# Kernel optimization log

Measured on AMD Instinct MI355X. Metric: run time of the kernel, lower is better.

## Reference

```python
import jax, jax.numpy as jnp
import numpy as np

B, D, NH, HD, L, P, FF = 2, 256, 8, 32, 4, 4, 1024
SPATIAL = np.array([[100, 100], [50, 50], [25, 25], [13, 13]], dtype=np.int64)
S_TOTAL = int(SPATIAL.prod(1).sum())  # 13294
EPS = 1e-5


def setup_inputs() -> dict:
    key = jax.random.key(0)
    ks = jax.random.split(key, 20)
    std = 0.02
    f32 = jnp.float32
    return {
        "query": jax.random.normal(ks[0], (B, S_TOTAL, D), f32),
        "query_pos": jax.random.normal(ks[1], (B, S_TOTAL, D), f32),
        "valid_ratios": jnp.ones((B, L, 2), f32),
        "spatial_shapes": SPATIAL,
        "level_start_index": np.concatenate([[0], SPATIAL.prod(1).cumsum()[:-1]]).astype(np.int64),
        "W_off": jax.random.normal(ks[2], (D, NH * L * P * 2), f32) * std,
        "b_off": jax.random.normal(ks[3], (NH * L * P * 2,), f32) * std,
        "W_attn": jax.random.normal(ks[4], (D, NH * L * P), f32) * std,
        "b_attn": jax.random.normal(ks[5], (NH * L * P,), f32) * std,
        "W_val": jax.random.normal(ks[6], (D, D), f32) * std,
        "b_val": jnp.zeros((D,), f32),
        "W_out": jax.random.normal(ks[7], (D, D), f32) * std,
        "b_out": jnp.zeros((D,), f32),
        "ln1_g": jnp.ones((D,), f32),
        "ln1_b": jnp.zeros((D,), f32),
        "W1": jax.random.normal(ks[8], (D, FF), f32) * std,
        "b1": jnp.zeros((FF,), f32),
        "W2": jax.random.normal(ks[9], (FF, D), f32) * std,
        "b2": jnp.zeros((D,), f32),
        "ln2_g": jnp.ones((D,), f32),
        "ln2_b": jnp.zeros((D,), f32),
    }


def _layer_norm(x, g, b):
    m = x.mean(-1, keepdims=True)
    v = ((x - m) ** 2).mean(-1, keepdims=True)
    return (x - m) * jax.lax.rsqrt(v + EPS) * g + b


def _bilinear_sample(v, loc, H, W):
    # v: [B, NH, H*W, HD]; loc: [B, NH, S, P, 2] normalized to [0,1]
    # Matches F.grid_sample(bilinear, padding_mode='zeros', align_corners=False)
    x = loc[..., 0] * W - 0.5
    y = loc[..., 1] * H - 0.5
    x0 = jnp.floor(x)
    y0 = jnp.floor(y)
    lx, ly = x - x0, y - y0
    x0i = x0.astype(jnp.int32)
    y0i = y0.astype(jnp.int32)
    x1i, y1i = x0i + 1, y0i + 1

    def corner(yi, xi, w):
        valid = (xi >= 0) & (xi < W) & (yi >= 0) & (yi < H)
        idx = jnp.clip(yi, 0, H - 1) * W + jnp.clip(xi, 0, W - 1)  # [B,NH,S,P]
        b_, h_, s_, p_ = idx.shape
        g = jnp.take_along_axis(v, idx.reshape(b_, h_, s_ * p_)[..., None], axis=2)
        g = g.reshape(b_, h_, s_, p_, -1)
        return g * (w * valid)[..., None]

    return (corner(y0i, x0i, (1 - lx) * (1 - ly)) + corner(y0i, x1i, lx * (1 - ly))
            + corner(y1i, x0i, (1 - lx) * ly) + corner(y1i, x1i, lx * ly))


def _forward(query, query_pos, valid_ratios, spatial_shapes,
             W_off, b_off, W_attn, b_attn, W_val, b_val, W_out, b_out,
             ln1_g, ln1_b, W1, b1, W2, b2, ln2_g, ln2_b):
    ss = np.asarray(spatial_shapes)
    Bq, S, _ = query.shape

    # ----- reference points (per-pixel centers, normalized by valid ratios) -----
    refs = []
    for lvl in range(ss.shape[0]):
        H, W = int(ss[lvl, 0]), int(ss[lvl, 1])
        ry, rx = jnp.meshgrid(jnp.linspace(0.5, H - 0.5, H), jnp.linspace(0.5, W - 0.5, W), indexing='ij')
        vy = valid_ratios[:, lvl, 1][:, None, None]
        vx = valid_ratios[:, lvl, 0][:, None, None]
        ry = ry[None] / (vy * H)
        rx = rx[None] / (vx * W)
        refs.append(jnp.stack((rx, ry), -1).reshape(Bq, H * W, 2))
    ref = jnp.concatenate(refs, 1)  # [B, S, 2] (identical across levels)

    # ----- multi-scale deformable attention -----
    q = query + query_pos
    v = (query @ W_val + b_val).reshape(Bq, S, NH, HD).transpose(0, 2, 1, 3)  # [B,NH,S,HD]
    off = (q @ W_off + b_off).reshape(Bq, S, NH, L, P, 2)
    aw = jax.nn.softmax((q @ W_attn + b_attn).reshape(Bq, S, NH, L * P), -1)
    aw = aw.reshape(Bq, S, NH, L, P)
    normalizer = jnp.asarray(ss[:, ::-1].copy(), jnp.float32)  # (W, H) per level
    loc = ref[:, :, None, None, None, :] + off / normalizer[None, None, None, :, None, :]  # [B,S,NH,L,P,2]

    starts = np.concatenate([[0], ss.prod(1).cumsum()[:-1]])
    out = jnp.zeros((Bq, NH, S, HD), query.dtype)
    for lvl in range(ss.shape[0]):
        H, W = int(ss[lvl, 0]), int(ss[lvl, 1])
        s0 = int(starts[lvl])
        v_l = v[:, :, s0:s0 + H * W]                       # [B,NH,HW,HD]
        loc_l = loc[:, :, :, lvl].transpose(0, 2, 1, 3, 4)  # [B,NH,S,P,2]
        samp = _bilinear_sample(v_l, loc_l, H, W)           # [B,NH,S,P,HD]
        w_l = aw[:, :, :, lvl].transpose(0, 2, 1, 3)        # [B,NH,S,P]
        out = out + (samp * w_l[..., None]).sum(3)
    attn_out = out.transpose(0, 2, 1, 3).reshape(Bq, S, D) @ W_out + b_out

    # ----- residual + LN + FFN + residual + LN -----
    x = _layer_norm(query + attn_out, ln1_g, ln1_b)
    f = jax.nn.relu(x @ W1 + b1) @ W2 + b2
    return _layer_norm(x + f, ln2_g, ln2_b)


def reference(query, query_pos, valid_ratios, spatial_shapes, level_start_index,
              W_off, b_off, W_attn, b_attn, W_val, b_val, W_out, b_out,
              ln1_g, ln1_b, W1, b1, W2, b2, ln2_g, ln2_b):
    return _forward(query, query_pos, valid_ratios, spatial_shapes,
                    W_off, b_off, W_attn, b_attn, W_val, b_val, W_out, b_out,
                    ln1_g, ln1_b, W1, b1, W2, b2, ln2_g, ln2_b)
```

## Files before the change

kernel.cpp:

```cpp
#include <hip/hip_runtime.h>
#include <math.h>

#define R_ROWS 26588
#define S_TOT  13294
#define NHEAD  8
#define NLVL   4
#define EPSF   1e-5f

typedef __attribute__((ext_vector_type(8))) short short8;
typedef __attribute__((ext_vector_type(4))) float f32x4;
typedef __attribute__((ext_vector_type(2))) float f32x2;
typedef unsigned short ushort_t;

__device__ __forceinline__ unsigned short f2bf(float f) {
    unsigned int u = __builtin_bit_cast(unsigned int, f);
    unsigned int r = (u + 0x7FFFu + ((u >> 16) & 1u)) >> 16;
    return (unsigned short)r;
}

__global__ __launch_bounds__(256) void transpose_all_kernel(
    const float* __restrict__ W_val, const float* __restrict__ W_off,
    const float* __restrict__ W_attn, const float* __restrict__ W_out,
    const float* __restrict__ W1, const float* __restrict__ W2,
    ushort_t* __restrict__ wt_val, ushort_t* __restrict__ wt_off,
    ushort_t* __restrict__ wt_attn, ushort_t* __restrict__ wt_out,
    ushort_t* __restrict__ wt_w1, ushort_t* __restrict__ wt_w2)
{
    int bid = blockIdx.x;
    const float* src; ushort_t* dst; int K, N, t;
    if (bid < 64)       { src = W_val;  dst = wt_val;  K = 256;  N = 256;  t = bid; }
    else if (bid < 128) { src = W_off;  dst = wt_off;  K = 256;  N = 256;  t = bid - 64; }
    else if (bid < 160) { src = W_attn; dst = wt_attn; K = 256;  N = 128;  t = bid - 128; }
    else if (bid < 224) { src = W_out;  dst = wt_out;  K = 256;  N = 256;  t = bid - 160; }
    else if (bid < 480) { src = W1;     dst = wt_w1;   K = 256;  N = 1024; t = bid - 224; }
    else                { src = W2;     dst = wt_w2;   K = 1024; N = 256;  t = bid - 480; }
    int nt = N / 32;
    int bn = (t % nt) * 32, bk = (t / nt) * 32;

    __shared__ ushort_t tt[32][33];
    int x = threadIdx.x & 31;
    int y = threadIdx.x >> 5;
#pragma unroll
    for (int i = 0; i < 4; ++i) {
        int k = y + i * 8;
        tt[x][k] = f2bf(src[(long)(bk + k) * N + bn + x]);
    }
    __syncthreads();
#pragma unroll
    for (int i = 0; i < 4; ++i) {
        int n = y + i * 8;
        dst[(long)(bn + n) * K + bk + x] = tt[n][x];
    }
}

__global__ __launch_bounds__(256) void addcvt_kernel(
    const float* __restrict__ q, const float* __restrict__ p,
    ushort_t* __restrict__ qry_bf, ushort_t* __restrict__ qsum_bf, int n4)
{
    int i = blockIdx.x * 256 + threadIdx.x;
    if (i >= n4) return;
    float4 a = ((const float4*)q)[i];
    float4 b = ((const float4*)p)[i];
    uint2 qa, qs;
    qa.x = (unsigned)f2bf(a.x) | ((unsigned)f2bf(a.y) << 16);
    qa.y = (unsigned)f2bf(a.z) | ((unsigned)f2bf(a.w) << 16);
    qs.x = (unsigned)f2bf(a.x + b.x) | ((unsigned)f2bf(a.y + b.y) << 16);
    qs.y = (unsigned)f2bf(a.z + b.z) | ((unsigned)f2bf(a.w + b.w) << 16);
    ((uint2*)qry_bf)[i] = qa;
    ((uint2*)qsum_bf)[i] = qs;
}

__device__ __forceinline__ void gemm_body(
    ushort_t (*As)[40], ushort_t (*Bs)[40],
    const ushort_t* __restrict__ A, const ushort_t* __restrict__ Wt,
    const float* __restrict__ bias, void* __restrict__ Cv,
    int M, int N, int K, int bm, int bn, bool out_bf16, bool relu)
{
    const int tid  = threadIdx.x;
    const int wave = tid >> 6;
    const int lane = tid & 63;
    const int l15  = lane & 15;
    const int quad = lane >> 4;
    const int wm   = (wave >> 1) * 64;
    const int wn   = (wave & 1) * 64;
    const int kq   = (tid & 3) * 8;
    const int r0   = tid >> 2;

    f32x4 acc[4][4];
#pragma unroll
    for (int i = 0; i < 4; ++i)
#pragma unroll
        for (int j = 0; j < 4; ++j) acc[i][j] = (f32x4)0.0f;

    for (int k0 = 0; k0 < K; k0 += 32) {
#pragma unroll
        for (int i = 0; i < 2; ++i) {
            int r = r0 + i * 64;
            int m = bm + r;
            uint4 val; val.x = val.y = val.z = val.w = 0u;
            if (m < M) val = *(const uint4*)&A[(long)m * K + k0 + kq];
            *(uint4*)&As[r][kq] = val;
        }
#pragma unroll
        for (int i = 0; i < 2; ++i) {
            int n = r0 + i * 64;
            *(uint4*)&Bs[n][kq] = *(const uint4*)&Wt[(long)(bn + n) * K + k0 + kq];
        }
        __syncthreads();

        short8 af[4], bf[4];
#pragma unroll
        for (int mi = 0; mi < 4; ++mi)
            af[mi] = *(const short8*)&As[wm + mi * 16 + l15][quad * 8];
#pragma unroll
        for (int ni = 0; ni < 4; ++ni)
            bf[ni] = *(const short8*)&Bs[wn + ni * 16 + l15][quad * 8];
#pragma unroll
        for (int mi = 0; mi < 4; ++mi)
#pragma unroll
            for (int ni = 0; ni < 4; ++ni)
                acc[mi][ni] = __builtin_amdgcn_mfma_f32_16x16x32_bf16(
                    af[mi], bf[ni], acc[mi][ni], 0, 0, 0);
        __syncthreads();
    }

#pragma unroll
    for (int mi = 0; mi < 4; ++mi) {
#pragma unroll
        for (int r = 0; r < 4; ++r) {
            int row = bm + wm + mi * 16 + quad * 4 + r;
            if (row >= M) continue;
#pragma unroll
            for (int ni = 0; ni < 4; ++ni) {
                int col = bn + wn + ni * 16 + l15;
                float vv = acc[mi][ni][r] + bias[col];
                if (relu) vv = fmaxf(vv, 0.f);
                if (out_bf16)
                    ((ushort_t*)Cv)[(long)row * N + col] = f2bf(vv);
                else
                    ((float*)Cv)[(long)row * N + col] = vv;
            }
        }
    }
}

template<bool OUT_BF16, bool RELU>
__global__ __launch_bounds__(256) void gemm_mfma_kernel(
    const ushort_t* __restrict__ A, const ushort_t* __restrict__ Wt,
    const float* __restrict__ bias, void* __restrict__ Cv,
    int M, int N, int K)
{
    __shared__ ushort_t As[128][40];
    __shared__ ushort_t Bs[128][40];
    gemm_body(As, Bs, A, Wt, bias, Cv, M, N, K,
              blockIdx.x * 128, blockIdx.y * 128, OUT_BF16, RELU);
}

__global__ __launch_bounds__(256) void proj_kernel(
    const ushort_t* __restrict__ qry_bf, const ushort_t* __restrict__ q_bf,
    const ushort_t* __restrict__ wt_val, const ushort_t* __restrict__ wt_off,
    const ushort_t* __restrict__ wt_attn,
    const float* __restrict__ b_val, const float* __restrict__ b_off,
    const float* __restrict__ b_attn,
    ushort_t* __restrict__ v_bf, float* __restrict__ cb, float* __restrict__ logits)
{
    __shared__ ushort_t As[128][40];
    __shared__ ushort_t Bs[128][40];
    int y = blockIdx.y;
    const ushort_t* A; const ushort_t* Wt; const float* bias;
    void* C; bool outbf; int N, bn;
    if (y < 2)      { A = qry_bf; Wt = wt_val;  bias = b_val;  C = v_bf;   outbf = true;  N = 256; bn = y * 128; }
    else if (y < 4) { A = q_bf;   Wt = wt_off;  bias = b_off;  C = cb;     outbf = false; N = 256; bn = (y - 2) * 128; }
    else            { A = q_bf;   Wt = wt_attn; bias = b_attn; C = logits; outbf = false; N = 128; bn = 0; }
    gemm_body(As, Bs, A, Wt, bias, C, R_ROWS, N, 256, blockIdx.x * 128, bn, outbf, false);
}

__global__ __launch_bounds__(256) void deform_sample_kernel(
    const ushort_t* __restrict__ v, const float* __restrict__ off,
    const float* __restrict__ logits, const float* __restrict__ vr,
    ushort_t* __restrict__ out)
{
    const int Hs_[4] = {100, 50, 25, 13};
    const int S0_[4] = {0, 10000, 12500, 13125};

    int grp = blockIdx.x * 64 + (threadIdx.x >> 2);
    int j   = threadIdx.x & 3;
    if (grp >= R_ROWS * NHEAD) return;
    int h = grp & 7;
    int r = grp >> 3;
    int b = (r >= S_TOT) ? 1 : 0;
    int s = r - b * S_TOT;

    int lq = (s < 10000) ? 0 : (s < 12500) ? 1 : (s < 13125) ? 2 : 3;
    int t  = s - S0_[lq];
    int Wq = Hs_[lq];
    int iy = t / Wq;
    int jx = t - iy * Wq;
    float vx = vr[(b * NLVL + lq) * 2 + 0];
    float vy = vr[(b * NLVL + lq) * 2 + 1];
    float rx = (jx + 0.5f) / (vx * (float)Wq);
    float ry = (iy + 0.5f) / (vy * (float)Wq);

    const float* offp = off + (long)r * 256 + h * 32;
    float4 oa = ((const float4*)offp)[2 * j];
    float4 ob = ((const float4*)offp)[2 * j + 1];
    float4 lg = ((const float4*)(logits + (long)grp * 16))[j];

    float mx = fmaxf(fmaxf(lg.x, lg.y), fmaxf(lg.z, lg.w));
    mx = fmaxf(mx, __shfl_xor(mx, 1));
    mx = fmaxf(mx, __shfl_xor(mx, 2));
    float e0 = __expf(lg.x - mx), e1 = __expf(lg.y - mx);
    float e2 = __expf(lg.z - mx), e3 = __expf(lg.w - mx);
    float sum = e0 + e1 + e2 + e3;
    sum += __shfl_xor(sum, 1);
    sum += __shfl_xor(sum, 2);
    float inv = 1.f / sum;

    const int   H  = Hs_[j];
    const float fH = (float)H;
    const int   s0 = S0_[j];
    float oxs[4] = {oa.x, oa.z, ob.x, ob.z};
    float oys[4] = {oa.y, oa.w, ob.y, ob.w};
    float wts[4] = {e0 * inv, e1 * inv, e2 * inv, e3 * inv};
    float pw0[4], pw1[4], pw2[4], pw3[4];
    int   pi0[4], pi1[4], pi2[4], pi3[4];
#pragma unroll
    for (int i = 0; i < 4; ++i) {
        float x = rx * fH + oxs[i] - 0.5f;
        float y = ry * fH + oys[i] - 0.5f;
        float xf = floorf(x), yf = floorf(y);
        float lx = x - xf, ly = y - yf;
        int x0 = (int)xf, y0 = (int)yf;
        bool xv0 = (x0 >= 0) & (x0 < H);
        bool xv1 = (x0 >= -1) & (x0 < H - 1);
        bool yv0 = (y0 >= 0) & (y0 < H);
        bool yv1 = (y0 >= -1) & (y0 < H - 1);
        float w = wts[i];
        pw0[i] = (xv0 & yv0) ? (1.f - lx) * (1.f - ly) * w : 0.f;
        pw1[i] = (xv1 & yv0) ? lx * (1.f - ly) * w : 0.f;
        pw2[i] = (xv0 & yv1) ? (1.f - lx) * ly * w : 0.f;
        pw3[i] = (xv1 & yv1) ? lx * ly * w : 0.f;
        int xc0 = min(max(x0, 0), H - 1), xc1 = min(max(x0 + 1, 0), H - 1);
        int yc0 = min(max(y0, 0), H - 1), yc1 = min(max(y0 + 1, 0), H - 1);
        pi0[i] = s0 + yc0 * H + xc0;
        pi1[i] = s0 + yc0 * H + xc1;
        pi2[i] = s0 + yc1 * H + xc0;
        pi3[i] = s0 + yc1 * H + xc1;
    }

    const ushort_t* vb = v + ((long)b * S_TOT) * 256 + h * 32 + j * 8;
    f32x2 acc2[4];
#pragma unroll
    for (int c = 0; c < 4; ++c) acc2[c] = (f32x2)0.0f;

#define ACC_CORNER(IDX, WGT) do {                                            \
        uint4 g = *(const uint4*)&vb[(long)(IDX) * 256];                     \
        unsigned uu0 = g.x, uu1 = g.y, uu2 = g.z, uu3 = g.w;                 \
        f32x2 gv;                                                            \
        gv.x = __builtin_bit_cast(float, uu0 << 16);                         \
        gv.y = __builtin_bit_cast(float, uu0 & 0xFFFF0000u);                 \
        acc2[0] += gv * (WGT);                                               \
        gv.x = __builtin_bit_cast(float, uu1 << 16);                         \
        gv.y = __builtin_bit_cast(float, uu1 & 0xFFFF0000u);                 \
        acc2[1] += gv * (WGT);                                               \
        gv.x = __builtin_bit_cast(float, uu2 << 16);                         \
        gv.y = __builtin_bit_cast(float, uu2 & 0xFFFF0000u);                 \
        acc2[2] += gv * (WGT);                                               \
        gv.x = __builtin_bit_cast(float, uu3 << 16);                         \
        gv.y = __builtin_bit_cast(float, uu3 & 0xFFFF0000u);                 \
        acc2[3] += gv * (WGT);                                               \
    } while (0)

#pragma unroll
    for (int i = 0; i < 4; ++i) {
#pragma unroll
        for (int j2 = 0; j2 < 4; ++j2) {
            float w00 = __shfl(pw0[i], j2, 4);
            float w01 = __shfl(pw1[i], j2, 4);
            float w10 = __shfl(pw2[i], j2, 4);
            float w11 = __shfl(pw3[i], j2, 4);
            int   i00 = __shfl(pi0[i], j2, 4);
            int   i01 = __shfl(pi1[i], j2, 4);
            int   i10 = __shfl(pi2[i], j2, 4);
            int   i11 = __shfl(pi3[i], j2, 4);
            ACC_CORNER(i00, w00);
            ACC_CORNER(i01, w01);
            ACC_CORNER(i10, w10);
            ACC_CORNER(i11, w11);
        }
    }
#undef ACC_CORNER

    uint4 o;
    o.x = (unsigned)f2bf(acc2[0].x) | ((unsigned)f2bf(acc2[0].y) << 16);
    o.y = (unsigned)f2bf(acc2[1].x) | ((unsigned)f2bf(acc2[1].y) << 16);
    o.z = (unsigned)f2bf(acc2[2].x) | ((unsigned)f2bf(acc2[2].y) << 16);
    o.w = (unsigned)f2bf(acc2[3].x) | ((unsigned)f2bf(acc2[3].y) << 16);
    *(uint4*)&out[(long)r * 256 + h * 32 + j * 8] = o;
}

template<bool DUAL>
__global__ __launch_bounds__(256) void add_ln_kernel(
    const float* __restrict__ a, const float* __restrict__ b,
    const float* __restrict__ g, const float* __restrict__ beta,
    float* __restrict__ outf, ushort_t* __restrict__ outb)
{
    int row = blockIdx.x;
    int tid = threadIdx.x;
    float x = a[(long)row * 256 + tid] + b[(long)row * 256 + tid];
    float s1 = x, s2 = x * x;
#pragma unroll
    for (int o = 32; o > 0; o >>= 1) {
        s1 += __shfl_down(s1, o, 64);
        s2 += __shfl_down(s2, o, 64);
    }
    __shared__ float sh1[4], sh2[4];
    int w = tid >> 6;
    if ((tid & 63) == 0) { sh1[w] = s1; sh2[w] = s2; }
    __syncthreads();
    float t1 = sh1[0] + sh1[1] + sh1[2] + sh1[3];
    float t2 = sh2[0] + sh2[1] + sh2[2] + sh2[3];
    float mean = t1 * (1.f / 256.f);
    float var  = t2 * (1.f / 256.f) - mean * mean;
    float inv  = rsqrtf(var + EPSF);
    float y = (x - mean) * inv * g[tid] + beta[tid];
    outf[(long)row * 256 + tid] = y;
    if (DUAL) outb[(long)row * 256 + tid] = f2bf(y);
}

extern "C" void kernel_launch(void* const* d_in, const int* in_sizes, int n_in,
                              void* d_out, int out_size, void* d_ws, size_t ws_size,
                              hipStream_t stream)
{
    const float* query  = (const float*)d_in[0];
    const float* qpos   = (const float*)d_in[1];
    const float* vr     = (const float*)d_in[2];
    const float* W_off  = (const float*)d_in[5];
    const float* b_off  = (const float*)d_in[6];
    const float* W_attn = (const float*)d_in[7];
    const float* b_attn = (const float*)d_in[8];
    const float* W_val  = (const float*)d_in[9];
    const float* b_val  = (const float*)d_in[10];
    const float* W_out  = (const float*)d_in[11];
    const float* b_out  = (const float*)d_in[12];
    const float* ln1g   = (const float*)d_in[13];
    const float* ln1b   = (const float*)d_in[14];
    const float* W1     = (const float*)d_in[15];
    const float* b1     = (const float*)d_in[16];
    const float* W2     = (const float*)d_in[17];
    const float* b2     = (const float*)d_in[18];
    const float* ln2g   = (const float*)d_in[19];
    const float* ln2b   = (const float*)d_in[20];
    float* out = (float*)d_out;

    float* ws = (float*)d_ws;
    const long R128 = (long)R_ROWS * 128;
    ushort_t* q_bf    = (ushort_t*)(ws);
    ushort_t* qry_bf  = (ushort_t*)(ws + R128);
    ushort_t* v_bf    = (ushort_t*)(ws + 2 * R128);
    float*    logits  = ws + 3 * R128;
    ushort_t* h_bf    = (ushort_t*)(ws);
    float*    cb      = ws + 4 * R128;
    ushort_t* samp_bf = (ushort_t*)(ws + 6 * R128);
    float*    xb      = ws + 7 * R128;
    ushort_t* wt      = (ushort_t*)(ws + 9 * R128);
    ushort_t* wt_val  = wt;
    ushort_t* wt_off  = wt + 65536;
    ushort_t* wt_attn = wt + 131072;
    ushort_t* wt_out  = wt + 163840;
    ushort_t* wt_w1   = wt + 229376;
    ushort_t* wt_w2   = wt + 491520;

    dim3 blk(256);
    const int MB = (R_ROWS + 127) / 128;

    transpose_all_kernel<<<736, blk, 0, stream>>>(
        W_val, W_off, W_attn, W_out, W1, W2,
        wt_val, wt_off, wt_attn, wt_out, wt_w1, wt_w2);
    addcvt_kernel<<<(R_ROWS * 64 + 255) / 256, blk, 0, stream>>>(
        query, qpos, qry_bf, q_bf, R_ROWS * 64);
    proj_kernel<<<dim3(MB, 5), blk, 0, stream>>>(
        qry_bf, q_bf, wt_val, wt_off, wt_attn, b_val, b_off, b_attn,
        v_bf, cb, logits);
    deform_sample_kernel<<<(R_ROWS * NHEAD + 63) / 64, blk, 0, stream>>>(
        v_bf, cb, logits, vr, samp_bf);
    gemm_mfma_kernel<false, false><<<dim3(MB, 2), blk, 0, stream>>>(
        samp_bf, wt_out, b_out, cb, R_ROWS, 256, 256);
    add_ln_kernel<true><<<R_ROWS, blk, 0, stream>>>(query, cb, ln1g, ln1b, xb, samp_bf);
    gemm_mfma_kernel<true, true><<<dim3(MB, 8), blk, 0, stream>>>(
        samp_bf, wt_w1, b1, h_bf, R_ROWS, 1024, 256);
    gemm_mfma_kernel<false, false><<<dim3(MB, 2), blk, 0, stream>>>(
        h_bf, wt_w2, b2, cb, R_ROWS, 256, 1024);
    add_ln_kernel<false><<<R_ROWS, blk, 0, stream>>>(xb, cb, ln2g, ln2b, out, nullptr);
}
```

Before: 344.9 us.

## Stage GEMM tiles with direct global-to-LDS loads and XOR-swizzled layout

```diff
diff --git a/kernel.cpp b/kernel.cpp
--- a/kernel.cpp
+++ b/kernel.cpp
@@ -70,8 +70,26 @@
     ((uint2*)qsum_bf)[i] = qs;
 }
 
+__device__ __forceinline__ void stage32_async(
+    const ushort_t* __restrict__ src_row0, int ld, int k0,
+    ushort_t* lds, int wave, int lane)
+{
+#pragma unroll
+    for (int inst = 0; inst < 2; ++inst) {
+        int base_row = wave * 32 + inst * 16;
+        int r = base_row + (lane >> 2);
+        int quadS = lane & 3;
+        int quadG = quadS ^ ((r >> 1) & 3);
+        const ushort_t* gp = src_row0 + (long)r * ld + k0 + quadG * 8;
+        __builtin_amdgcn_global_load_lds(
+            (const __attribute__((address_space(1))) unsigned int*)gp,
+            (__attribute__((address_space(3))) unsigned int*)&lds[base_row * 32],
+            16, 0, 0);
+    }
+}
+
 __device__ __forceinline__ void gemm_body(
-    ushort_t (*As)[40], ushort_t (*Bs)[40],
+    ushort_t* As, ushort_t* Bs,
     const ushort_t* __restrict__ A, const ushort_t* __restrict__ Wt,
     const float* __restrict__ bias, void* __restrict__ Cv,
     int M, int N, int K, int bm, int bn, bool out_bf16, bool relu)
@@ -83,8 +101,9 @@
     const int quad = lane >> 4;
     const int wm   = (wave >> 1) * 64;
     const int wn   = (wave & 1) * 64;
-    const int kq   = (tid & 3) * 8;
-    const int r0   = tid >> 2;
+
+    const ushort_t* Arow = A + (long)bm * K;
+    const ushort_t* Brow = Wt + (long)bn * K;
 
     f32x4 acc[4][4];
 #pragma unroll
@@ -92,29 +111,28 @@
 #pragma unroll
         for (int j = 0; j < 4; ++j) acc[i][j] = (f32x4)0.0f;
 
+    int aoff[4], boff[4];
+#pragma unroll
+    for (int mi = 0; mi < 4; ++mi) {
+        int r = wm + mi * 16 + l15;
+        aoff[mi] = r * 32 + (quad ^ ((r >> 1) & 3)) * 8;
+    }
+#pragma unroll
+    for (int ni = 0; ni < 4; ++ni) {
+        int r = wn + ni * 16 + l15;
+        boff[ni] = r * 32 + (quad ^ ((r >> 1) & 3)) * 8;
+    }
+
     for (int k0 = 0; k0 < K; k0 += 32) {
-#pragma unroll
-        for (int i = 0; i < 2; ++i) {
-            int r = r0 + i * 64;
-            int m = bm + r;
-            uint4 val; val.x = val.y = val.z = val.w = 0u;
-            if (m < M) val = *(const uint4*)&A[(long)m * K + k0 + kq];
-            *(uint4*)&As[r][kq] = val;
-        }
-#pragma unroll
-        for (int i = 0; i < 2; ++i) {
-            int n = r0 + i * 64;
-            *(uint4*)&Bs[n][kq] = *(const uint4*)&Wt[(long)(bn + n) * K + k0 + kq];
-        }
+        stage32_async(Arow, K, k0, As, wave, lane);
+        stage32_async(Brow, K, k0, Bs, wave, lane);
         __syncthreads();
 
         short8 af[4], bf[4];
 #pragma unroll
-        for (int mi = 0; mi < 4; ++mi)
-            af[mi] = *(const short8*)&As[wm + mi * 16 + l15][quad * 8];
-#pragma unroll
-        for (int ni = 0; ni < 4; ++ni)
-            bf[ni] = *(const short8*)&Bs[wn + ni * 16 + l15][quad * 8];
+        for (int mi = 0; mi < 4; ++mi) af[mi] = *(const short8*)&As[aoff[mi]];
+#pragma unroll
+        for (int ni = 0; ni < 4; ++ni) bf[ni] = *(const short8*)&Bs[boff[ni]];
 #pragma unroll
         for (int mi = 0; mi < 4; ++mi)
 #pragma unroll
@@ -150,8 +168,8 @@
     const float* __restrict__ bias, void* __restrict__ Cv,
     int M, int N, int K)
 {
-    __shared__ ushort_t As[128][40];
-    __shared__ ushort_t Bs[128][40];
+    __shared__ ushort_t As[128 * 32];
+    __shared__ ushort_t Bs[128 * 32];
     gemm_body(As, Bs, A, Wt, bias, Cv, M, N, K,
               blockIdx.x * 128, blockIdx.y * 128, OUT_BF16, RELU);
 }
@@ -164,8 +182,8 @@
     const float* __restrict__ b_attn,
     ushort_t* __restrict__ v_bf, float* __restrict__ cb, float* __restrict__ logits)
 {
-    __shared__ ushort_t As[128][40];
-    __shared__ ushort_t Bs[128][40];
+    __shared__ ushort_t As[128 * 32];
+    __shared__ ushort_t Bs[128 * 32];
     int y = blockIdx.y;
     const ushort_t* A; const ushort_t* Wt; const float* bias;
     void* C; bool outbf; int N, bn;
```

Result: faster. 333.4 us (-3.3%).
